# Kernel optimization log

Measured on AMD Instinct MI355X. Metric: run time of the kernel, lower is better.

The kernel has to match this reference:

```python
import jax, jax.numpy as jnp
import numpy as np

NUM_HEADS = 16
NEG = -10000000.0


def setup_inputs() -> dict:
    key = jax.random.key(0)
    k1, k2, k3 = jax.random.split(key, 3)
    B, N, C = 4, 2048, 1024
    inputs = jax.random.normal(k1, (B, N, C), dtype=jnp.float32)
    # learned params (xavier-ish scale)
    W_qkv = jax.random.normal(k2, (C, 3 * C), dtype=jnp.float32) * 0.02
    W_proj = jax.random.normal(k3, (C, C), dtype=jnp.float32) * 0.02
    b_proj = jnp.zeros((C,), dtype=jnp.float32)
    attn_mask = jnp.ones((N, N), dtype=jnp.int32)      # >0 means keep
    padding_mask = jnp.zeros((B, N), dtype=jnp.int32)  # >0 means mask out
    return {"inputs": inputs, "attn_mask": attn_mask, "padding_mask": padding_mask,
            "W_qkv": W_qkv, "W_proj": W_proj, "b_proj": b_proj}


def reference(inputs, attn_mask, padding_mask, W_qkv, W_proj, b_proj):
    B, N, C = inputs.shape
    H = NUM_HEADS
    d = C // H
    scale = d ** -0.5
    qkv = inputs @ W_qkv                                   # [B,N,3C]
    qkv = qkv.reshape(B, N, 3, H, d).transpose(2, 0, 3, 1, 4)  # [3,B,H,N,d]
    q, k, v = qkv[0], qkv[1], qkv[2]
    scores = jnp.einsum('bhqd,bhkd->bhqk', q, k) * scale   # [B,H,N,N]
    scores = jnp.where(attn_mask > 0, scores, NEG)
    pm = padding_mask[:, None, None, :]                    # [B,1,1,N]
    scores = jnp.where(pm > 0, NEG, scores)
    attn = jax.nn.softmax(scores, axis=-1)
    x = jnp.einsum('bhqk,bhkd->bhqd', attn, v)             # [B,H,N,d]
    x = x.swapaxes(1, 2).reshape(B, N, C)
    return x @ W_proj + b_proj
```

## Files before the change

### kernel.cpp

```cpp
#include <hip/hip_runtime.h>

#define NEG -10000000.0f
#define QSCALE 0.18033688011112042f

typedef __attribute__((ext_vector_type(8))) short bf16x8;
typedef __attribute__((ext_vector_type(4))) float f32x4;

static __device__ __forceinline__ short f2bf(float f) {
    unsigned int u = __float_as_uint(f);
    unsigned int r = (u + 0x7fffu + ((u >> 16) & 1u)) >> 16;
    return (short)r;
}

static __device__ __forceinline__ unsigned pack_bf16_2(float a, float b) {
    unsigned ua = __float_as_uint(a) + 0x8000u;
    unsigned ub = __float_as_uint(b) + 0x8000u;
    return __builtin_amdgcn_perm(ub, ua, 0x07060302u);
}

static __device__ __forceinline__ void async_cp16(const void* g, void* l) {
    __builtin_amdgcn_global_load_lds(
        (const __attribute__((address_space(1))) unsigned int*)g,
        (__attribute__((address_space(3))) unsigned int*)l, 16, 0, 0);
}

__global__ void cvt_bf16(const float* __restrict__ src, short* __restrict__ dst, int n4) {
    int i = blockIdx.x * blockDim.x + threadIdx.x;
    if (i < n4) {
        float4 v = reinterpret_cast<const float4*>(src)[i];
        short4 o;
        o.x = f2bf(v.x); o.y = f2bf(v.y); o.z = f2bf(v.z); o.w = f2bf(v.w);
        reinterpret_cast<short4*>(dst)[i] = o;
    }
}

__global__ void transpose_cvt(const float* __restrict__ src, short* __restrict__ dst,
                              int rows, int cols) {
    __shared__ float tile[32][33];
    int bx = blockIdx.x * 32;
    int by = blockIdx.y * 32;
    int tx = threadIdx.x & 31, ty = threadIdx.x >> 5;
    for (int j = 0; j < 4; ++j)
        tile[ty + j * 8][tx] = src[(size_t)(by + ty + j * 8) * cols + bx + tx];
    __syncthreads();
    for (int j = 0; j < 4; ++j)
        dst[(size_t)(bx + ty + j * 8) * rows + by + tx] = f2bf(tile[tx][ty + j * 8]);
}

__global__ void mask_flags(const int* __restrict__ attn_mask, int* __restrict__ flags) {
    int blk = blockIdx.x;
    int qt = blk >> 5, kt = blk & 31;
    int tid = threadIdx.x;
    __shared__ int blockok;
    if (tid == 0) blockok = 1;
    __syncthreads();
    int ok = 1;
    for (int j = 0; j < 32; ++j) {
        int idx = j * 256 + tid;
        int qr = qt * 128 + (idx >> 6);
        int kc = kt * 64 + (idx & 63);
        ok &= (attn_mask[(size_t)qr * 2048 + kc] != 0);
    }
    if (!ok) blockok = 0;
    __syncthreads();
    if (tid == 0) flags[blk] = blockok;
}

__global__ void pad_flags(const int* __restrict__ padding, int* __restrict__ pf) {
    int t = threadIdx.x;
    int b = t >> 5, kt = t & 31;
    int any = 0;
    for (int j = 0; j < 64; ++j) any |= (padding[b * 2048 + kt * 64 + j] > 0);
    pf[t] = any;
}

__global__ __launch_bounds__(256, 2) void gemm_bf16(
    const short* __restrict__ A, const short* __restrict__ Bt, int mode,
    short* __restrict__ q_ws, short* __restrict__ k_ws, short* __restrict__ v_ws,
    float* __restrict__ out, const float* __restrict__ bias) {
    const int K = 1024;
    __shared__ __align__(16) short smem[2][128][64];
    short (*As)[64] = smem[0];
    short (*Bs)[64] = smem[1];
    int tid = threadIdx.x, lane = tid & 63, w = tid >> 6;
    int wm = w & 1, wn = w >> 1;
    int m0 = blockIdx.y * 128, n0 = blockIdx.x * 128;
    int col = lane & 15, quad = lane >> 4;
    int l8 = lane >> 3, j8 = lane & 7;

    f32x4 acc[4][4] = {};

    for (int k0 = 0; k0 < K; k0 += 64) {
        for (int c = 0; c < 4; ++c) {
            int rr = w * 32 + c * 8 + l8;
            int sw = (j8 ^ (rr & 7)) << 3;
            async_cp16(&A[(size_t)(m0 + rr) * K + k0 + sw], &As[w * 32 + c * 8][0]);
            async_cp16(&Bt[(size_t)(n0 + rr) * K + k0 + sw], &Bs[w * 32 + c * 8][0]);
        }
        __syncthreads();
        for (int ks = 0; ks < 2; ++ks) {
            bf16x8 af[4], bfr[4];
            for (int mt = 0; mt < 4; ++mt)
                af[mt] = *reinterpret_cast<const bf16x8*>(
                    &As[wm * 64 + mt * 16 + col][((ks * 4 + quad) ^ (col & 7)) << 3]);
            for (int nt = 0; nt < 4; ++nt)
                bfr[nt] = *reinterpret_cast<const bf16x8*>(
                    &Bs[wn * 64 + nt * 16 + col][((ks * 4 + quad) ^ (col & 7)) << 3]);
            for (int mt = 0; mt < 4; ++mt)
                for (int nt = 0; nt < 4; ++nt)
                    acc[mt][nt] = __builtin_amdgcn_mfma_f32_16x16x32_bf16(af[mt], bfr[nt], acc[mt][nt], 0, 0, 0);
        }
        __syncthreads();
    }

    short* L = &smem[0][0][0];

    if (mode == 0) {
        int which = n0 >> 10;
        int cb = n0 & 1023;
        int b = m0 >> 11, nb = m0 & 2047, hb = cb >> 6;
        if (which == 2) {
            for (int mt = 0; mt < 4; ++mt)
                for (int nt = 0; nt < 4; ++nt) {
                    int ml = wm * 64 + mt * 16 + quad * 4;
                    int cl = wn * 64 + nt * 16 + col;
                    int mp = (ml + 8 * cl) & 127;
                    short4 pk;
                    for (int r = 0; r < 4; ++r) ((short*)&pk)[r] = f2bf(acc[mt][nt][r]);
                    *reinterpret_cast<short4*>(&L[cl * 128 + mp]) = pk;
                }
            __syncthreads();
            for (int it = 0; it < 8; ++it) {
                int chunk = it * 256 + tid;
                int c = chunk >> 4, j = chunk & 15;
                int h = hb + (c >> 6), dd = c & 63;
                int4 val = *reinterpret_cast<const int4*>(&L[c * 128 + (((j + c) & 15) << 3)]);
                *reinterpret_cast<int4*>(
                    &v_ws[((size_t)((b * 16 + h) * 64 + dd)) * 2048 + nb + j * 8]) = val;
            }
        } else {
            short* dst = (which == 0) ? q_ws : k_ws;
            float scl = (which == 0) ? QSCALE : 1.0f;
            for (int mt = 0; mt < 4; ++mt)
                for (int nt = 0; nt < 4; ++nt)
                    for (int r = 0; r < 4; ++r) {
                        int ml = wm * 64 + mt * 16 + quad * 4 + r;
                        int cl = wn * 64 + nt * 16 + col;
                        L[ml * 128 + ((cl + 8 * ml) & 127)] = f2bf(acc[mt][nt][r] * scl);
                    }
            __syncthreads();
            for (int it = 0; it < 8; ++it) {
                int chunk = it * 256 + tid;
                int row = chunk >> 4, j = chunk & 15;
                int h = hb + (j >> 3), dd = (j & 7) * 8;
                int4 val = *reinterpret_cast<const int4*>(&L[row * 128 + (((j + row) & 15) << 3)]);
                *reinterpret_cast<int4*>(
                    &dst[((size_t)(b * 16 + h) * 2048 + nb + row) * 64 + dd]) = val;
            }
        }
    } else {
        float* Lf = reinterpret_cast<float*>(L);
        for (int half = 0; half < 2; ++half) {
            if (wm == half) {
                for (int mt = 0; mt < 4; ++mt)
                    for (int nt = 0; nt < 4; ++nt)
                        for (int r = 0; r < 4; ++r) {
                            int ml = mt * 16 + quad * 4 + r;
                            int cl = wn * 64 + nt * 16 + col;
                            Lf[ml * 128 + cl] = acc[mt][nt][r];
                        }
            }
            __syncthreads();
            for (int it = 0; it < 8; ++it) {
                int chunk = it * 256 + tid;
                int row = chunk >> 5, j = chunk & 31;
                float4 val = *reinterpret_cast<const float4*>(&Lf[row * 128 + j * 4]);
                float4 bv = *reinterpret_cast<const float4*>(&bias[n0 + j * 4]);
                val.x += bv.x; val.y += bv.y; val.z += bv.z; val.w += bv.w;
                *reinterpret_cast<float4*>(
                    &out[(size_t)(m0 + half * 64 + row) * 1024 + n0 + j * 4]) = val;
            }
            __syncthreads();
        }
    }
}

__global__ __launch_bounds__(256, 4) void flash_attn(
    const short* __restrict__ q_ws, const short* __restrict__ k_ws,
    const short* __restrict__ v_ws, const int* __restrict__ aflags,
    const int* __restrict__ pflags, const int* __restrict__ padding,
    const int* __restrict__ attn_mask, short* __restrict__ xb) {
    const int Nn = 2048, D = 64;
    __shared__ short QP[128][64];
    __shared__ short Ks[64][64];
    __shared__ short Vt[64][64];
    __shared__ __align__(16) float padb[64];

    int tid = threadIdx.x, lane = tid & 63, w = tid >> 6;
    int col = lane & 15, quad = lane >> 4;
    int bh = blockIdx.y, b = bh >> 4, h = bh & 15;
    int q0 = blockIdx.x * 128, qt = blockIdx.x;
    int l8 = lane >> 3, j8 = lane & 7;

    for (int c = 0; c < 4; ++c) {
        int rr = w * 32 + c * 8 + l8;
        async_cp16(&q_ws[((size_t)bh * Nn + q0 + rr) * D + ((j8 ^ (rr & 7)) << 3)],
                   &QP[w * 32 + c * 8][0]);
    }
    __syncthreads();

    bf16x8 qf[2][2];
    for (int t = 0; t < 2; ++t)
        for (int ks = 0; ks < 2; ++ks)
            qf[t][ks] = *reinterpret_cast<const bf16x8*>(
                &QP[w * 32 + t * 16 + col][((ks * 4 + quad) ^ (col & 7)) << 3]);

    f32x4 oacc[2][4] = {};
    f32x4 lacc[2] = {};

    for (int kt = 0; kt < 32; ++kt) {
        int k0 = kt * 64;
        for (int c = 0; c < 2; ++c) {
            int rr = w * 16 + c * 8 + l8;
            int sw = (j8 ^ (rr & 7)) << 3;
            async_cp16(&k_ws[((size_t)bh * Nn + k0 + rr) * D + sw], &Ks[w * 16 + c * 8][0]);
            async_cp16(&v_ws[((size_t)bh * D + rr) * Nn + k0 + sw], &Vt[w * 16 + c * 8][0]);
        }
        int pflag = pflags[b * 32 + kt];
        if (pflag && tid < 64) padb[tid] = (padding[b * Nn + k0 + tid] > 0) ? NEG : 0.f;
        __syncthreads();

        f32x4 sacc[4][2] = {};
        for (int ks = 0; ks < 2; ++ks) {
            bf16x8 kf[4];
            for (int mt = 0; mt < 4; ++mt)
                kf[mt] = *reinterpret_cast<const bf16x8*>(
                    &Ks[mt * 16 + col][((ks * 4 + quad) ^ (col & 7)) << 3]);
            for (int mt = 0; mt < 4; ++mt)
                for (int t = 0; t < 2; ++t)
                    sacc[mt][t] = __builtin_amdgcn_mfma_f32_16x16x32_bf16(kf[mt], qf[t][ks], sacc[mt][t], 0, 0, 0);
        }

        if (!aflags[qt * 32 + kt]) {
            for (int mt = 0; mt < 4; ++mt)
                for (int t = 0; t < 2; ++t)
                    for (int r = 0; r < 4; ++r) {
                        int kc = k0 + mt * 16 + quad * 4 + r;
                        int qr = q0 + w * 32 + t * 16 + col;
                        if (attn_mask[(size_t)qr * Nn + kc] == 0) sacc[mt][t][r] = NEG;
                    }
        }
        if (pflag) {
            for (int mt = 0; mt < 4; ++mt) {
                f32x4 pb = *reinterpret_cast<const f32x4*>(&padb[mt * 16 + quad * 4]);
                for (int t = 0; t < 2; ++t)
                    for (int r = 0; r < 4; ++r) sacc[mt][t][r] += pb[r];
            }
        }

        for (int t = 0; t < 2; ++t) {
            int qrow = w * 32 + t * 16 + col;
            for (int mt = 0; mt < 4; ++mt) {
                f32x4 e;
                e[0] = __builtin_amdgcn_exp2f(sacc[mt][t][0]);
                e[1] = __builtin_amdgcn_exp2f(sacc[mt][t][1]);
                e[2] = __builtin_amdgcn_exp2f(sacc[mt][t][2]);
                e[3] = __builtin_amdgcn_exp2f(sacc[mt][t][3]);
                lacc[t] += e;
                unsigned p0 = pack_bf16_2(e[0], e[1]);
                unsigned p1 = pack_bf16_2(e[2], e[3]);
                int chunk = (mt * 2 + (quad >> 1)) ^ (col & 7);
                *reinterpret_cast<uint2*>(&QP[qrow][(chunk << 3) + ((quad & 1) << 2)]) =
                    make_uint2(p0, p1);
            }
        }

        for (int ks = 0; ks < 2; ++ks) {
            bf16x8 pf[2], vf[4];
            for (int t = 0; t < 2; ++t)
                pf[t] = *reinterpret_cast<const bf16x8*>(
                    &QP[w * 32 + t * 16 + col][((ks * 4 + quad) ^ (col & 7)) << 3]);
            for (int nt = 0; nt < 4; ++nt)
                vf[nt] = *reinterpret_cast<const bf16x8*>(
                    &Vt[nt * 16 + col][((ks * 4 + quad) ^ (col & 7)) << 3]);
            for (int t = 0; t < 2; ++t)
                for (int nt = 0; nt < 4; ++nt)
                    oacc[t][nt] = __builtin_amdgcn_mfma_f32_16x16x32_bf16(pf[t], vf[nt], oacc[t][nt], 0, 0, 0);
        }
        __syncthreads();
    }

    for (int t = 0; t < 2; ++t) {
        float ls = lacc[t][0] + lacc[t][1] + lacc[t][2] + lacc[t][3];
        ls += __shfl_xor(ls, 16);
        ls += __shfl_xor(ls, 32);
        for (int r = 0; r < 4; ++r) {
            float lv = __shfl(ls, quad * 4 + r, 16);
            float inv = 1.f / lv;
            int n = q0 + w * 32 + t * 16 + quad * 4 + r;
            for (int nt = 0; nt < 4; ++nt) {
                int dd = nt * 16 + col;
                xb[((size_t)(b * Nn + n)) * 1024 + h * 64 + dd] = f2bf(oacc[t][nt][r] * inv);
            }
        }
    }
}

extern "C" void kernel_launch(void* const* d_in, const int* in_sizes, int n_in,
                              void* d_out, int out_size, void* d_ws, size_t ws_size,
                              hipStream_t stream) {
    const float* x        = (const float*)d_in[0];
    const int* attn_mask  = (const int*)d_in[1];
    const int* padding    = (const int*)d_in[2];
    const float* W_qkv    = (const float*)d_in[3];
    const float* W_proj   = (const float*)d_in[4];
    const float* b_proj   = (const float*)d_in[5];
    float* out            = (float*)d_out;

    char* ws = (char*)d_ws;
    short* Xb   = (short*)(ws);
    short* Wqt  = (short*)(ws + (16u << 20));
    short* Wpt  = (short*)(ws + (22u << 20));
    short* q_ws = (short*)(ws + (24u << 20));
    short* k_ws = (short*)(ws + (40u << 20));
    short* v_ws = (short*)(ws + (56u << 20));
    short* xbuf = (short*)(ws + (72u << 20));
    int*  flags = (int*)(ws + (88u << 20));

    cvt_bf16<<<8192, 256, 0, stream>>>(x, Xb, 8388608 / 4);
    transpose_cvt<<<dim3(3072 / 32, 1024 / 32), 256, 0, stream>>>(W_qkv, Wqt, 1024, 3072);
    transpose_cvt<<<dim3(1024 / 32, 1024 / 32), 256, 0, stream>>>(W_proj, Wpt, 1024, 1024);
    mask_flags<<<512, 256, 0, stream>>>(attn_mask, flags);
    pad_flags<<<1, 128, 0, stream>>>(padding, flags + 512);

    gemm_bf16<<<dim3(3072 / 128, 8192 / 128), 256, 0, stream>>>(
        Xb, Wqt, 0, q_ws, k_ws, v_ws, nullptr, nullptr);

    flash_attn<<<dim3(16, 64), 256, 0, stream>>>(
        q_ws, k_ws, v_ws, flags, flags + 512, padding, attn_mask, xbuf);

    gemm_bf16<<<dim3(1024 / 128, 8192 / 128), 256, 0, stream>>>(
        xbuf, Wpt, 1, nullptr, nullptr, nullptr, out, b_proj);
}
```

Before: 297.2 us.

## Double-buffer K tiles and prefetch V asynchronously in flash attention loop

Restructures the flash attention key loop into a software pipeline. K tiles are double-buffered and the next K tile is issued right after the QK MFMAs. The next V tile is loaded into the single V buffer after the PV MFMAs, with fine-grained vmcnt waits and raw barriers replacing full __syncthreads. Mask flags are preloaded into wave ballot bitmasks, padding bias is read directly from global memory instead of through LDS, and MFMA sections get raised wave priority. This aims to hide global-to-LDS latency behind compute, at the cost of more LDS, more complex synchronization, and risk of ordering hazards.

After: 327.1 us. +10.1%, slower.

```diff
diff --git a/kernel.cpp b/kernel.cpp
--- a/kernel.cpp
+++ b/kernel.cpp
@@ -191,10 +191,9 @@
     const int* __restrict__ pflags, const int* __restrict__ padding,
     const int* __restrict__ attn_mask, short* __restrict__ xb) {
     const int Nn = 2048, D = 64;
-    __shared__ short QP[128][64];
-    __shared__ short Ks[64][64];
-    __shared__ short Vt[64][64];
-    __shared__ __align__(16) float padb[64];
+    __shared__ __align__(16) short QP[128][64];
+    __shared__ __align__(16) short Ks[2][64][64];
+    __shared__ __align__(16) short Vt[64][64];
 
     int tid = threadIdx.x, lane = tid & 63, w = tid >> 6;
     int col = lane & 15, quad = lane >> 4;
@@ -202,10 +201,21 @@
     int q0 = blockIdx.x * 128, qt = blockIdx.x;
     int l8 = lane >> 3, j8 = lane & 7;
 
+    unsigned amask = (unsigned)__ballot(aflags[qt * 32 + (lane & 31)] != 0);
+    unsigned pmask = (unsigned)__ballot(pflags[b * 32 + (lane & 31)] != 0);
+
     for (int c = 0; c < 4; ++c) {
         int rr = w * 32 + c * 8 + l8;
         async_cp16(&q_ws[((size_t)bh * Nn + q0 + rr) * D + ((j8 ^ (rr & 7)) << 3)],
                    &QP[w * 32 + c * 8][0]);
+    }
+    {
+        int rr0 = w * 16 + l8, rr1 = w * 16 + 8 + l8;
+        int s0 = (j8 ^ (rr0 & 7)) << 3, s1 = (j8 ^ (rr1 & 7)) << 3;
+        async_cp16(&k_ws[((size_t)bh * Nn + rr0) * D + s0], &Ks[0][w * 16][0]);
+        async_cp16(&k_ws[((size_t)bh * Nn + rr1) * D + s1], &Ks[0][w * 16 + 8][0]);
+        async_cp16(&v_ws[((size_t)bh * D + rr0) * Nn + s0], &Vt[w * 16][0]);
+        async_cp16(&v_ws[((size_t)bh * D + rr1) * Nn + s1], &Vt[w * 16 + 8][0]);
     }
     __syncthreads();
 
@@ -220,28 +230,36 @@
 
     for (int kt = 0; kt < 32; ++kt) {
         int k0 = kt * 64;
-        for (int c = 0; c < 2; ++c) {
-            int rr = w * 16 + c * 8 + l8;
-            int sw = (j8 ^ (rr & 7)) << 3;
-            async_cp16(&k_ws[((size_t)bh * Nn + k0 + rr) * D + sw], &Ks[w * 16 + c * 8][0]);
-            async_cp16(&v_ws[((size_t)bh * D + rr) * Nn + k0 + sw], &Vt[w * 16 + c * 8][0]);
-        }
-        int pflag = pflags[b * 32 + kt];
-        if (pflag && tid < 64) padb[tid] = (padding[b * Nn + k0 + tid] > 0) ? NEG : 0.f;
-        __syncthreads();
+        int ktn = (kt < 31) ? kt + 1 : 31;
+
+        if (kt) {
+            asm volatile("s_waitcnt vmcnt(2)" ::: "memory");
+            __builtin_amdgcn_s_barrier();
+            __builtin_amdgcn_sched_barrier(0);
+        }
+        const short (*Kc)[64] = Ks[kt & 1];
 
         f32x4 sacc[4][2] = {};
         for (int ks = 0; ks < 2; ++ks) {
             bf16x8 kf[4];
             for (int mt = 0; mt < 4; ++mt)
                 kf[mt] = *reinterpret_cast<const bf16x8*>(
-                    &Ks[mt * 16 + col][((ks * 4 + quad) ^ (col & 7)) << 3]);
+                    &Kc[mt * 16 + col][((ks * 4 + quad) ^ (col & 7)) << 3]);
+            __builtin_amdgcn_s_setprio(1);
             for (int mt = 0; mt < 4; ++mt)
                 for (int t = 0; t < 2; ++t)
                     sacc[mt][t] = __builtin_amdgcn_mfma_f32_16x16x32_bf16(kf[mt], qf[t][ks], sacc[mt][t], 0, 0, 0);
-        }
-
-        if (!aflags[qt * 32 + kt]) {
+            __builtin_amdgcn_s_setprio(0);
+        }
+
+        {
+            int rr0 = w * 16 + l8, rr1 = w * 16 + 8 + l8;
+            size_t kb = (size_t)bh * Nn + ktn * 64;
+            async_cp16(&k_ws[(kb + rr0) * D + ((j8 ^ (rr0 & 7)) << 3)], &Ks[(kt + 1) & 1][w * 16][0]);
+            async_cp16(&k_ws[(kb + rr1) * D + ((j8 ^ (rr1 & 7)) << 3)], &Ks[(kt + 1) & 1][w * 16 + 8][0]);
+        }
+
+        if (!((amask >> kt) & 1)) {
             for (int mt = 0; mt < 4; ++mt)
                 for (int t = 0; t < 2; ++t)
                     for (int r = 0; r < 4; ++r) {
@@ -250,12 +268,13 @@
                         if (attn_mask[(size_t)qr * Nn + kc] == 0) sacc[mt][t][r] = NEG;
                     }
         }
-        if (pflag) {
-            for (int mt = 0; mt < 4; ++mt) {
-                f32x4 pb = *reinterpret_cast<const f32x4*>(&padb[mt * 16 + quad * 4]);
-                for (int t = 0; t < 2; ++t)
-                    for (int r = 0; r < 4; ++r) sacc[mt][t][r] += pb[r];
-            }
+        if ((pmask >> kt) & 1) {
+            for (int mt = 0; mt < 4; ++mt)
+                for (int r = 0; r < 4; ++r) {
+                    int kc = k0 + mt * 16 + quad * 4 + r;
+                    float pb = (padding[b * Nn + kc] > 0) ? NEG : 0.f;
+                    for (int t = 0; t < 2; ++t) sacc[mt][t][r] += pb;
+                }
         }
 
         for (int t = 0; t < 2; ++t) {
@@ -275,6 +294,12 @@
             }
         }
 
+        if (kt) {
+            asm volatile("s_waitcnt vmcnt(2)" ::: "memory");
+            __builtin_amdgcn_s_barrier();
+            __builtin_amdgcn_sched_barrier(0);
+        }
+
         for (int ks = 0; ks < 2; ++ks) {
             bf16x8 pf[2], vf[4];
             for (int t = 0; t < 2; ++t)
@@ -283,11 +308,23 @@
             for (int nt = 0; nt < 4; ++nt)
                 vf[nt] = *reinterpret_cast<const bf16x8*>(
                     &Vt[nt * 16 + col][((ks * 4 + quad) ^ (col & 7)) << 3]);
+            __builtin_amdgcn_s_setprio(1);
             for (int t = 0; t < 2; ++t)
                 for (int nt = 0; nt < 4; ++nt)
                     oacc[t][nt] = __builtin_amdgcn_mfma_f32_16x16x32_bf16(pf[t], vf[nt], oacc[t][nt], 0, 0, 0);
-        }
-        __syncthreads();
+            __builtin_amdgcn_s_setprio(0);
+        }
+
+        asm volatile("s_waitcnt lgkmcnt(0)" ::: "memory");
+        __builtin_amdgcn_sched_barrier(0);
+        __builtin_amdgcn_s_barrier();
+        {
+            int rr0 = w * 16 + l8, rr1 = w * 16 + 8 + l8;
+            size_t vb0 = ((size_t)bh * D + rr0) * Nn + ktn * 64;
+            size_t vb1 = ((size_t)bh * D + rr1) * Nn + ktn * 64;
+            async_cp16(&v_ws[vb0 + ((j8 ^ (rr0 & 7)) << 3)], &Vt[w * 16][0]);
+            async_cp16(&v_ws[vb1 + ((j8 ^ (rr1 & 7)) << 3)], &Vt[w * 16 + 8][0]);
+        }
     }
 
     for (int t = 0; t < 2; ++t) {
```
